# Optimization experiments

Measured on AMD Instinct MI355X. Metric: run time of the kernel, lower is better.

The kernel has to match this reference:

```python
import jax, jax.numpy as jnp
import numpy as np

CHUNK = 64  # triangles processed per scan step; [CHUNK, S*S] intermediates (~64MB fp32)


def setup_inputs() -> dict:
    key = jax.random.key(0)
    kv, kf = jax.random.split(key)
    N, T = 10000, 2048
    vertices = jax.random.normal(kv, (N, 3), dtype=jnp.float32)
    faces = jax.random.randint(kf, (T, 3), 0, N)
    return {"vertices": vertices, "faces": faces, "elevation": 30, "azimuth": 45, "image_size": 500}


def _forward(vertices, faces, elevation, azimuth, image_size):
    S = int(image_size)
    deg = jnp.float32(np.pi / 180.0)
    e = jnp.float32(elevation) * deg
    a = jnp.float32(azimuth) * deg
    ca, sa, ce, se = jnp.cos(a), jnp.sin(a), jnp.cos(e), jnp.sin(e)
    rot_y = jnp.array([[ca, 0.0, sa], [0.0, 1.0, 0.0], [-sa, 0.0, ca]], dtype=jnp.float32)
    rot_x = jnp.array([[1.0, 0.0, 0.0], [0.0, ce, -se], [0.0, se, ce]], dtype=jnp.float32)
    vr = vertices @ (rot_y @ rot_x)                     # [N,3] rotated
    vr = vr.at[:, 2].add(2.0)                           # push in front of camera
    v2d = vr[:, :2] / vr[:, 2:3]                        # perspective divide
    v2d = (v2d + 1.0) * (S / 2.0)                       # NDC -> pixel coords

    f0, f1, f2 = faces[:, 0], faces[:, 1], faces[:, 2]
    p0, p1, p2 = vr[f0], vr[f1], vr[f2]
    n = jnp.cross(p1 - p0, p2 - p0)
    n = n / (jnp.linalg.norm(n, axis=1, keepdims=True) + 1e-8)
    diffuse = jnp.clip(n[:, 2], 0.0, 1.0) * 180.0 + 75.0        # light_dir = (0,0,1)
    colors = jnp.broadcast_to(diffuse[:, None], (faces.shape[0], 3)).astype(jnp.float32)

    z = vr[:, 2][faces].mean(axis=1)                    # [T] painter depth

    tri = jnp.trunc(v2d[faces])                         # [T,3,2]; matches torch .long() truncation
    V0, V1, V2 = tri[:, 0], tri[:, 1], tri[:, 2]
    area = 0.5 * jnp.abs((V1[:, 0] - V0[:, 0]) * (V2[:, 1] - V0[:, 1])
                         - (V2[:, 0] - V0[:, 0]) * (V1[:, 1] - V0[:, 1]))
    valid = area >= 1e-5

    # clamped bounding boxes (note: original never draws row/col image_size-1)
    mnx = jnp.maximum(0.0, jnp.min(tri[:, :, 0], 1))
    mxx = jnp.minimum(S - 1.0, jnp.max(tri[:, :, 0], 1) + 1.0)
    mny = jnp.maximum(0.0, jnp.min(tri[:, :, 1], 1))
    mxy = jnp.minimum(S - 1.0, jnp.max(tri[:, :, 1], 1) + 1.0)

    xs = jnp.arange(S, dtype=jnp.float32)
    gy, gx = jnp.meshgrid(xs, xs, indexing='ij')
    px, py = gx.reshape(-1), gy.reshape(-1)             # [P] pixel centers
    P = S * S
    T = faces.shape[0]
    pad = (-T) % CHUNK

    def padc(x, v):
        if pad == 0:
            return x
        return jnp.concatenate([x, jnp.full((pad,) + x.shape[1:], v, x.dtype)], axis=0)

    nch = (T + pad) // CHUNK

    def r(x):
        return x.reshape((nch, CHUNK) + x.shape[1:])

    chunks = (r(padc(tri, 0.0)), r(padc(colors, 0.0)), r(padc(z, np.inf)),
              r(padc(area, 0.0)), r(padc(valid, False)),
              r(padc(mnx, 0.0)), r(padc(mxx, 0.0)), r(padc(mny, 0.0)), r(padc(mxy, 0.0)))

    # Painter's algorithm (draw far->near, near overwrites) == per-pixel min-z covering triangle.
    def body(carry, c):
        bz, bc = carry
        t, col, zc, ar, vld, x0, x1, y0, y1 = c
        v0x, v0y = t[:, 0, 0][:, None], t[:, 0, 1][:, None]
        v1x, v1y = t[:, 1, 0][:, None], t[:, 1, 1][:, None]
        v2x, v2y = t[:, 2, 0][:, None], t[:, 2, 1][:, None]
        inv = (1.0 / (ar + 1e-8))[:, None]
        w0 = 0.5 * jnp.abs((v1x - px) * (v2y - py) - (v2x - px) * (v1y - py)) * inv
        w1 = 0.5 * jnp.abs((v2x - px) * (v0y - py) - (v0x - px) * (v2y - py)) * inv
        w2 = 1.0 - w0 - w1
        cover = (w0 >= 0) & (w1 >= 0) & (w2 >= 0) & (w0 <= 1) & (w1 <= 1) & (w2 <= 1)
        inbox = (px >= x0[:, None]) & (px < x1[:, None]) & (py >= y0[:, None]) & (py < y1[:, None])
        ok = cover & inbox & vld[:, None]                # [C,P]
        zeff = jnp.where(ok, zc[:, None], jnp.inf)
        zmin = jnp.min(zeff, axis=0)                     # [P]
        i = jnp.argmin(zeff, axis=0)                     # [P]
        cand = col[i]                                    # [P,3]
        upd = zmin < bz
        return (jnp.where(upd, zmin, bz), jnp.where(upd[:, None], cand, bc)), None

    init = (jnp.full((P,), np.inf, jnp.float32), jnp.full((P, 3), 255.0, jnp.float32))
    (bz, bc), _ = jax.lax.scan(body, init, chunks)
    return bc.reshape(S, S, 3)


def reference(vertices, faces, elevation, azimuth, image_size):
    return _forward(vertices, faces, elevation, azimuth, image_size)
```

## Files before the change

### kernel.cpp

```cpp
#include <hip/hip_runtime.h>
#include <math.h>


#define TILE 16
#define K    8

__device__ __forceinline__ void rot_matrix(int elev, int azim,
                                           float& r00, float& r01, float& r02,
                                           float& r11, float& r12,
                                           float& r20, float& r21, float& r22) {
  const float degf = (float)(3.14159265358979323846 / 180.0);
  float e = __fmul_rn((float)elev, degf);
  float a = __fmul_rn((float)azim, degf);
  float ca = (float)cos((double)a);
  float sa = (float)sin((double)a);
  float ce = (float)cos((double)e);
  float se = (float)sin((double)e);
  r00 = ca;  r01 = __fmul_rn(sa, se); r02 = __fmul_rn(sa, ce);
  r11 = ce;  r12 = -se;
  r20 = -sa; r21 = __fmul_rn(ca, se); r22 = __fmul_rn(ca, ce);
}

__device__ __forceinline__ void xform_vertex(
    const float* __restrict__ verts, int i, float halfS,
    float r00, float r01, float r02, float r11, float r12,
    float r20, float r21, float r22,
    float& X, float& Y, float& Z, float& TX, float& TY) {
  float a0 = verts[3 * i + 0];
  float a1 = verts[3 * i + 1];
  float a2 = verts[3 * i + 2];
  float x = __fadd_rn(__fadd_rn(__fmul_rn(a0, r00), __fmul_rn(a1, 0.0f)), __fmul_rn(a2, r20));
  float y = __fadd_rn(__fadd_rn(__fmul_rn(a0, r01), __fmul_rn(a1, r11)), __fmul_rn(a2, r21));
  float z = __fadd_rn(__fadd_rn(__fmul_rn(a0, r02), __fmul_rn(a1, r12)), __fmul_rn(a2, r22));
  z = __fadd_rn(z, 2.0f);
  float sx = __fmul_rn(__fadd_rn(__fdiv_rn(x, z), 1.0f), halfS);
  float sy = __fmul_rn(__fadd_rn(__fdiv_rn(y, z), 1.0f), halfS);
  X = x; Y = y; Z = z;
  TX = truncf(sx);
  TY = truncf(sy);
}

__global__ void prep_kernel(const int* __restrict__ faces,
                            const float* __restrict__ verts,
                            const int* __restrict__ elev,
                            const int* __restrict__ azim,
                            float4* __restrict__ rec,
                            float* __restrict__ gx0, float* __restrict__ gx1,
                            float* __restrict__ gy0, float* __restrict__ gy1,
                            float* __restrict__ gv0x, float* __restrict__ gv0y,
                            float* __restrict__ gv1x, float* __restrict__ gv1y,
                            float* __restrict__ gv2x, float* __restrict__ gv2y,
                            float* __restrict__ ginv, unsigned* __restrict__ gzu,
                            float* __restrict__ colors,
                            ulonglong2* __restrict__ keybuf2, int n2,
                            int T, const int* __restrict__ psize) {
  int t = blockIdx.x * blockDim.x + threadIdx.x;
  if (t < n2) keybuf2[t] = make_ulonglong2(~0ULL, ~0ULL);
  if (t >= T) return;
  float r00, r01, r02, r11, r12, r20, r21, r22;
  rot_matrix(*elev, *azim, r00, r01, r02, r11, r12, r20, r21, r22);
  int S = *psize;
  float halfS = (float)((double)S * 0.5);
  int f0 = faces[3 * t + 0];
  int f1 = faces[3 * t + 1];
  int f2 = faces[3 * t + 2];
  float p0x, p0y, p0z, t0x, t0y;
  float p1x, p1y, p1z, t1x, t1y;
  float p2x, p2y, p2z, t2x, t2y;
  xform_vertex(verts, f0, halfS, r00, r01, r02, r11, r12, r20, r21, r22,
               p0x, p0y, p0z, t0x, t0y);
  xform_vertex(verts, f1, halfS, r00, r01, r02, r11, r12, r20, r21, r22,
               p1x, p1y, p1z, t1x, t1y);
  xform_vertex(verts, f2, halfS, r00, r01, r02, r11, r12, r20, r21, r22,
               p2x, p2y, p2z, t2x, t2y);
  float e1x = __fsub_rn(p1x, p0x), e1y = __fsub_rn(p1y, p0y), e1z = __fsub_rn(p1z, p0z);
  float e2x = __fsub_rn(p2x, p0x), e2y = __fsub_rn(p2y, p0y), e2z = __fsub_rn(p2z, p0z);
  float nx = __fsub_rn(__fmul_rn(e1y, e2z), __fmul_rn(e1z, e2y));
  float ny = __fsub_rn(__fmul_rn(e1z, e2x), __fmul_rn(e1x, e2z));
  float nz = __fsub_rn(__fmul_rn(e1x, e2y), __fmul_rn(e1y, e2x));
  float nrm = __fsqrt_rn(__fadd_rn(__fadd_rn(__fmul_rn(nx, nx), __fmul_rn(ny, ny)),
                                   __fmul_rn(nz, nz)));
  float nnz = __fdiv_rn(nz, __fadd_rn(nrm, 1e-8f));
  float cl = fminf(fmaxf(nnz, 0.0f), 1.0f);
  float col = __fadd_rn(__fmul_rn(cl, 180.0f), 75.0f);
  float zf = __fdiv_rn(__fadd_rn(__fadd_rn(p0z, p1z), p2z), 3.0f);
  float cr = __fsub_rn(__fmul_rn(__fsub_rn(t1x, t0x), __fsub_rn(t2y, t0y)),
                       __fmul_rn(__fsub_rn(t2x, t0x), __fsub_rn(t1y, t0y)));
  float area = __fmul_rn(0.5f, fabsf(cr));
  bool valid = (area >= 1e-5f);
  float inv = __fdiv_rn(1.0f, __fadd_rn(area, 1e-8f));
  float Sm1 = (float)(S - 1);
  float x0 = fmaxf(0.0f, fminf(fminf(t0x, t1x), t2x));
  float x1 = fminf(Sm1, __fadd_rn(fmaxf(fmaxf(t0x, t1x), t2x), 1.0f));
  float y0 = fmaxf(0.0f, fminf(fminf(t0y, t1y), t2y));
  float y1 = fminf(Sm1, __fadd_rn(fmaxf(fmaxf(t0y, t1y), t2y), 1.0f));
  unsigned zb = __float_as_uint(zf);
  unsigned zu = (zb & 0x80000000u) ? ~zb : (zb | 0x80000000u);
  if (!valid) x1 = -3.0e38f;
  gx0[t] = x0; gx1[t] = x1; gy0[t] = y0; gy1[t] = y1;
  gv0x[t] = t0x; gv0y[t] = t0y;
  gv1x[t] = t1x; gv1y[t] = t1y;
  gv2x[t] = t2x; gv2y[t] = t2y;
  ginv[t] = inv;
  gzu[t] = zu;
  colors[t] = col;
  float4 r0, r1, r2, r3;
  r0.x = t0x; r0.y = t0y; r0.z = t1x; r0.w = t1y;
  r1.x = t2x; r1.y = t2y; r1.z = x0;  r1.w = x1;
  r2.x = y0;  r2.y = y1;  r2.z = inv; r2.w = col;
  r3.x = __uint_as_float(zu); r3.y = __uint_as_float((unsigned)t);
  r3.z = 0.0f; r3.w = 0.0f;
  rec[4 * t + 0] = r0;
  rec[4 * t + 1] = r1;
  rec[4 * t + 2] = r2;
  rec[4 * t + 3] = r3;
}

__device__ __forceinline__ bool covers_rect(
    float q0x, float q0y, float q1x, float q1y, float q2x, float q2y,
    float qinv, float X0, float X1, float Y0, float Y1) {
  bool fin = fabsf(q0x) < 1e17f && fabsf(q0y) < 1e17f &&
             fabsf(q1x) < 1e17f && fabsf(q1y) < 1e17f &&
             fabsf(q2x) < 1e17f && fabsf(q2y) < 1e17f;
  if (!fin) return false;
  float A0 = q1x - X0, A1 = q1x - X1, B0 = q2y - Y0, B1 = q2y - Y1;
  float C0 = q2x - X0, C1 = q2x - X1, D0 = q1y - Y0, D1 = q1y - Y1;
  float E0 = q0y - Y0, E1 = q0y - Y1, F0 = q0x - X0, F1 = q0x - X1;
  float p, q;
  p = A0 * B0; q = C0 * D0; float u00 = p - q; float su = fabsf(p) + fabsf(q);
  p = A0 * B1; q = C0 * D1; float u01 = p - q; su = fmaxf(su, fabsf(p) + fabsf(q));
  p = A1 * B0; q = C1 * D0; float u10 = p - q; su = fmaxf(su, fabsf(p) + fabsf(q));
  p = A1 * B1; q = C1 * D1; float u11 = p - q; su = fmaxf(su, fabsf(p) + fabsf(q));
  p = C0 * E0; q = F0 * B0; float v00 = p - q; float sv = fabsf(p) + fabsf(q);
  p = C0 * E1; q = F0 * B1; float v01 = p - q; sv = fmaxf(sv, fabsf(p) + fabsf(q));
  p = C1 * E0; q = F1 * B0; float v10 = p - q; sv = fmaxf(sv, fabsf(p) + fabsf(q));
  p = C1 * E1; q = F1 * B1; float v11 = p - q; sv = fmaxf(sv, fabsf(p) + fabsf(q));
  float umax = fmaxf(fmaxf(fabsf(u00), fabsf(u01)), fmaxf(fabsf(u10), fabsf(u11)));
  float vmax = fmaxf(fmaxf(fabsf(v00), fabsf(v01)), fmaxf(fabsf(v10), fabsf(v11)));
  float epsU = 2e-6f * su, epsV = 2e-6f * sv;
  float hv = 0.5f * qinv;
  return ((umax + epsU) * hv <= 0.9999f) &&
         ((vmax + epsV) * hv <= 0.9999f) &&
         ((umax + vmax + epsU + epsV) * hv <= 0.9999f);
}

__global__ __launch_bounds__(256) void cull_kernel(
    const float* __restrict__ gx0, const float* __restrict__ gx1,
    const float* __restrict__ gy0, const float* __restrict__ gy1,
    const float* __restrict__ gv0x, const float* __restrict__ gv0y,
    const float* __restrict__ gv1x, const float* __restrict__ gv1y,
    const float* __restrict__ gv2x, const float* __restrict__ gv2y,
    const float* __restrict__ ginv, const unsigned* __restrict__ gzu,
    unsigned* __restrict__ stripzu, int T, int ntx) {
  __shared__ unsigned red[4];
  int tile = blockIdx.x;
  int tid = threadIdx.x;
  int lane = tid & 63;
  int wid = tid >> 6;
  int tx = tile % ntx, ty = tile / ntx;
  float TX0 = (float)(tx * TILE), TX1 = (float)(tx * TILE + TILE - 1);
  float TY0 = (float)(ty * TILE), TY1 = (float)(ty * TILE + TILE - 1);

  unsigned best = 0xFFFFFFFFu;
  for (int g = tid; g < T; g += 256) {
    unsigned zu = gzu[g];
    if (zu >= best) continue;
    float x0 = gx0[g], x1 = gx1[g], y0 = gy0[g], y1 = gy1[g];
    if (!(TX0 >= x0 && TX1 < x1 && TY0 >= y0 && TY1 < y1)) continue;
    if (covers_rect(gv0x[g], gv0y[g], gv1x[g], gv1y[g], gv2x[g], gv2y[g],
                    ginv[g], TX0, TX1, TY0, TY1))
      best = zu;
  }
  for (int o = 32; o > 0; o >>= 1)
    best = min(best, (unsigned)__shfl_down((int)best, o));
  if (lane == 0) red[wid] = best;
  __syncthreads();
  unsigned tilezu = min(min(red[0], red[1]), min(red[2], red[3]));

  float Y0 = (float)(ty * TILE + wid * 4), Y1 = Y0 + 3.0f;
  unsigned sbest = tilezu;
  for (int g = lane; g < T; g += 64) {
    unsigned zu = gzu[g];
    if (zu >= sbest) continue;
    float x0 = gx0[g], x1 = gx1[g], y0 = gy0[g], y1 = gy1[g];
    if (!(TX0 >= x0 && TX1 < x1 && Y0 >= y0 && Y1 < y1)) continue;
    if (covers_rect(gv0x[g], gv0y[g], gv1x[g], gv1y[g], gv2x[g], gv2y[g],
                    ginv[g], TX0, TX1, Y0, Y1))
      sbest = zu;
  }
  for (int o = 32; o > 0; o >>= 1)
    sbest = min(sbest, (unsigned)__shfl_down((int)sbest, o));
  if (lane == 0) stripzu[tile * 4 + wid] = sbest;
}

__global__ __launch_bounds__(256) void raster_kernel(
    const float4* __restrict__ rec,
    const float* __restrict__ gx0, const float* __restrict__ gx1,
    const float* __restrict__ gy0, const float* __restrict__ gy1,
    const float* __restrict__ gv0x, const float* __restrict__ gv0y,
    const float* __restrict__ gv1x, const float* __restrict__ gv1y,
    const float* __restrict__ gv2x, const float* __restrict__ gv2y,
    const float* __restrict__ ginv, const unsigned* __restrict__ gzu,
    const unsigned* __restrict__ stripzu,
    const int* __restrict__ psize,
    unsigned long long* __restrict__ keybuf,
    int T, int ntx, int fpb) {
  int S = *psize;
  int tile = blockIdx.x / K;
  int rseg = blockIdx.x - tile * K;
  int tx = tile % ntx, ty = tile / ntx;
  int tid = threadIdx.x;
  int lane = tid & 63;
  int wid = tid >> 6;
  int col = tid & (TILE - 1);
  int row = tid / TILE;
  int px_i = tx * TILE + col;
  int py_i = ty * TILE + row;
  float px = (float)px_i, py = (float)py_i;
  bool inimg = (px_i < S) && (py_i < S);
  unsigned long long bkey = ~0ULL;
  unsigned tzu = stripzu[tile * 4 + wid];
  float wxlo = (float)(tx * TILE), wxhi = (float)(tx * TILE + TILE - 1);
  float wylo = (float)(ty * TILE + wid * 4);
  float wyhi = wylo + 3.0f;

  int base = rseg * fpb;
  int lim = min(base + fpb, T);

  for (int g = base; g < lim; g += 64) {
    int fi = g + lane;
    bool in = fi < lim;
    float fx0 = in ? gx0[fi] : 3.0e38f;
    float fx1 = in ? gx1[fi] : -3.0e38f;
    float fy0 = in ? gy0[fi] : 3.0e38f;
    float fy1 = in ? gy1[fi] : -3.0e38f;
    unsigned fzu = in ? gzu[fi] : 0xFFFFFFFFu;
    bool ovb = (wxhi >= fx0) && (wxlo < fx1) && (wyhi >= fy0) && (wylo < fy1) &&
               (fzu <= tzu);
    bool ov = false;
    if (ovb) {
      float q0x = gv0x[fi], q0y = gv0y[fi];
      float q1x = gv1x[fi], q1y = gv1y[fi];
      float q2x = gv2x[fi], q2y = gv2y[fi];
      float qinv = ginv[fi];
      bool fin = fabsf(q0x) < 1e17f && fabsf(q0y) < 1e17f &&
                 fabsf(q1x) < 1e17f && fabsf(q1y) < 1e17f &&
                 fabsf(q2x) < 1e17f && fabsf(q2y) < 1e17f;
      float X0 = fmaxf(wxlo, fx0), X1 = fminf(wxhi, fx1);
      float Y0 = fmaxf(wylo, fy0), Y1 = fminf(wyhi, fy1);
      float A0 = q1x - X0, A1 = q1x - X1;
      float B0 = q2y - Y0, B1 = q2y - Y1;
      float C0 = q2x - X0, C1 = q2x - X1;
      float D0 = q1y - Y0, D1 = q1y - Y1;
      float E0 = q0y - Y0, E1 = q0y - Y1;
      float F0 = q0x - X0, F1 = q0x - X1;
      float p, q;
      p = A0 * B0; q = C0 * D0; float u00 = p - q; float su = fabsf(p) + fabsf(q);
      p = A0 * B1; q = C0 * D1; float u01 = p - q; su = fmaxf(su, fabsf(p) + fabsf(q));
      p = A1 * B0; q = C1 * D0; float u10 = p - q; su = fmaxf(su, fabsf(p) + fabsf(q));
      p = A1 * B1; q = C1 * D1; float u11 = p - q; su = fmaxf(su, fabsf(p) + fabsf(q));
      p = C0 * E0; q = F0 * B0; float v00 = p - q; float sv = fabsf(p) + fabsf(q);
      p = C0 * E1; q = F0 * B1; float v01 = p - q; sv = fmaxf(sv, fabsf(p) + fabsf(q));
      p = C1 * E0; q = F1 * B0; float v10 = p - q; sv = fmaxf(sv, fabsf(p) + fabsf(q));
      p = C1 * E1; q = F1 * B1; float v11 = p - q; sv = fmaxf(sv, fabsf(p) + fabsf(q));
      float epsU = 2e-6f * su;
      float epsV = 2e-6f * sv;
      float epsS = epsU + epsV;
      auto minabs4 = [](float x00, float x01, float x10, float x11, float eps) {
        float lo = fminf(fminf(x00, x01), fminf(x10, x11));
        float hi = fmaxf(fmaxf(x00, x01), fmaxf(x10, x11));
        float mres = 0.0f;
        if (lo > eps) mres = lo - eps;
        else if (hi < -eps) mres = -hi - eps;
        return mres;
      };
      float m0 = minabs4(u00, u01, u10, u11, epsU);
      float m1 = minabs4(v00, v01, v10, v11, epsV);
      float msum = minabs4(u00 + v00, u01 + v01, u10 + v10, u11 + v11, epsS);
      float mdif = minabs4(u00 - v00, u01 - v01, u10 - v10, u11 - v11, epsS);
      float mm = fmaxf(msum, mdif);
      float hv = 0.5f * qinv;
      bool rej = fin && ((m0 * hv > 1.0001f) || (m1 * hv > 1.0001f) ||
                         (mm * hv > 1.0001f));
      ov = !rej;
    }
    unsigned long long m = __ballot(ov);
    while (m) {
      int j0 = __builtin_ctzll(m); m &= m - 1;
      int j1 = -1, j2 = -1, j3 = -1;
      if (m) { j1 = __builtin_ctzll(m); m &= m - 1;
        if (m) { j2 = __builtin_ctzll(m); m &= m - 1;
          if (m) { j3 = __builtin_ctzll(m); m &= m - 1; } } }
      const float4* p0 = rec + 4 * (g + j0);
      const float4* p1 = rec + 4 * (g + (j1 >= 0 ? j1 : j0));
      const float4* p2 = rec + 4 * (g + (j2 >= 0 ? j2 : j0));
      const float4* p3 = rec + 4 * (g + (j3 >= 0 ? j3 : j0));
      float4 a0 = p0[0], a1 = p0[1], a2 = p0[2], a3 = p0[3];
      float4 b0 = p1[0], b1 = p1[1], b2 = p1[2], b3 = p1[3];
      float4 c0 = p2[0], c1 = p2[1], c2 = p2[2], c3 = p2[3];
      float4 d0 = p3[0], d1 = p3[1], d2 = p3[2], d3 = p3[3];

#define PROCESS(q0, q1, q2, q3, enable)                                        \
      if (enable) {                                                            \
        float v0x = q0.x, v0y = q0.y, v1x = q0.z, v1y = q0.w;                  \
        float v2x = q1.x, v2y = q1.y, x0 = q1.z, x1 = q1.w;                    \
        float y0 = q2.x, y1 = q2.y, inv = q2.z;                                \
                  \
        float e0 = __fsub_rn(__fmul_rn(__fsub_rn(v1x, px), __fsub_rn(v2y, py)),\
                             __fmul_rn(__fsub_rn(v2x, px), __fsub_rn(v1y, py)));\
        float w0 = __fmul_rn(__fmul_rn(0.5f, fabsf(e0)), inv);                 \
        float e1 = __fsub_rn(__fmul_rn(__fsub_rn(v2x, px), __fsub_rn(v0y, py)),\
                             __fmul_rn(__fsub_rn(v0x, px), __fsub_rn(v2y, py)));\
        float w1 = __fmul_rn(__fmul_rn(0.5f, fabsf(e1)), inv);                 \
        float w2 = __fsub_rn(__fsub_rn(1.0f, w0), w1);                         \
        bool ok = (w0 >= 0.0f) && (w1 >= 0.0f) && (w2 >= 0.0f) &&              \
                  (w0 <= 1.0f) && (w1 <= 1.0f) && (w2 <= 1.0f) &&              \
                  (px >= x0) && (px < x1) && (py >= y0) && (py < y1);          \
        unsigned long long fk =                                                \
            ((unsigned long long)__float_as_uint(q3.x) << 32) |                \
            __float_as_uint(q3.y);                                             \
        if (ok && fk < bkey) bkey = fk;                                        \
      }

      PROCESS(a0, a1, a2, a3, true)
      PROCESS(b0, b1, b2, b3, (j1 >= 0))
      PROCESS(c0, c1, c2, c3, (j2 >= 0))
      PROCESS(d0, d1, d2, d3, (j3 >= 0))
#undef PROCESS
    }
  }

  if (inimg && bkey != ~0ULL) {
    unsigned long long* kp = keybuf + ((size_t)py_i * (size_t)S + px_i);
    unsigned long long cur = *kp;
    if (bkey < cur) atomicMin(kp, bkey);
  }
}

__global__ void resolve_kernel(const unsigned long long* __restrict__ keybuf,
                               const float* __restrict__ colors,
                               float* __restrict__ out,
                               const int* __restrict__ psize) {
  int S = *psize;
  int P = S * S;
  int i = blockIdx.x * blockDim.x + threadIdx.x;
  if (i >= P) return;
  unsigned long long k = keybuf[i];
  float c = (k == 0xFFFFFFFFFFFFFFFFULL)
                ? 255.0f
                : colors[(unsigned)(k & 0xFFFFFFFFULL)];
  out[3 * i + 0] = c;
  out[3 * i + 1] = c;
  out[3 * i + 2] = c;
}

extern "C" void kernel_launch(void* const* d_in, const int* in_sizes, int n_in,
                              void* d_out, int out_size, void* d_ws, size_t ws_size,
                              hipStream_t stream) {
  const float* verts = (const float*)d_in[0];
  const int* faces = (const int*)d_in[1];
  const int* elev = (const int*)d_in[2];
  const int* azim = (const int*)d_in[3];
  const int* psize = (const int*)d_in[4];

  int T = in_sizes[1] / 3;
  const int S_host = 500;
  const int P = S_host * S_host;
  const int ntx = (S_host + TILE - 1) / TILE;
  const int nty = (S_host + TILE - 1) / TILE;
  const int ntiles = ntx * nty;
  int fpb = (((T + K - 1) / K + 63) / 64) * 64;

  float* wsf = (float*)d_ws;
  size_t off = 0;
  auto alloc = [&](size_t nfloats) {
    float* p = wsf + off;
    off += (nfloats + 15) & ~(size_t)15;
    return p;
  };
  float* gx0 = alloc(T);
  float* gx1 = alloc(T);
  float* gy0 = alloc(T);
  float* gy1 = alloc(T);
  float* gv0x = alloc(T);
  float* gv0y = alloc(T);
  float* gv1x = alloc(T);
  float* gv1y = alloc(T);
  float* gv2x = alloc(T);
  float* gv2y = alloc(T);
  float* ginv = alloc(T);
  unsigned* gzu = (unsigned*)alloc(T);
  float* colors = alloc(T);
  unsigned* stripzu = (unsigned*)alloc(ntiles * 4);
  float4* rec = (float4*)alloc((size_t)T * 16);
  unsigned long long* keybuf = (unsigned long long*)alloc((size_t)P * 2);

  int n2 = P / 2;
  int prep_threads = (n2 > T) ? n2 : T;
  prep_kernel<<<(prep_threads + 255) / 256, 256, 0, stream>>>(
      faces, verts, elev, azim, rec, gx0, gx1, gy0, gy1,
      gv0x, gv0y, gv1x, gv1y, gv2x, gv2y, ginv, gzu, colors,
      (ulonglong2*)keybuf, n2, T, psize);
  cull_kernel<<<ntiles, 256, 0, stream>>>(gx0, gx1, gy0, gy1,
                                          gv0x, gv0y, gv1x, gv1y, gv2x, gv2y,
                                          ginv, gzu, stripzu, T, ntx);
  raster_kernel<<<ntiles * K, 256, 0, stream>>>(rec, gx0, gx1, gy0, gy1,
                                                gv0x, gv0y, gv1x, gv1y, gv2x, gv2y,
                                                ginv, gzu, stripzu, psize, keybuf,
                                                T, ntx, fpb);
  resolve_kernel<<<(P + 255) / 256, 256, 0, stream>>>(keybuf, colors,
                                                      (float*)d_out, psize);
}
```

Baseline: 68.60 us.

## Map each wavefront to an 8x8 quad instead of a 16x4 strip, halve K

Each 64-lane wavefront now covers an 8x8 pixel quad of the 16x16 tile instead of a 16x4 row strip. The cull kernel computes a per-quad occluder depth to match. A square footprint overlaps fewer triangle bounding boxes and is more likely to be fully covered by an occluder, so fewer faces need per-pixel edge tests. Separately, the number of face segments per tile drops from 8 to 4, which halves the block count and gives each block more faces to scan. That lowers parallelism in exchange for fewer partial results per pixel.

Measured after the change: 68.21 us. About the same (-0.6%).

```diff
diff --git a/kernel.cpp b/kernel.cpp
--- a/kernel.cpp
+++ b/kernel.cpp
@@ -3,7 +3,7 @@
 
 
 #define TILE 16
-#define K    8
+#define K    4
 
 __device__ __forceinline__ void rot_matrix(int elev, int azim,
                                            float& r00, float& r01, float& r02,
@@ -151,7 +151,7 @@
     const float* __restrict__ gv1x, const float* __restrict__ gv1y,
     const float* __restrict__ gv2x, const float* __restrict__ gv2y,
     const float* __restrict__ ginv, const unsigned* __restrict__ gzu,
-    unsigned* __restrict__ stripzu, int T, int ntx) {
+    unsigned* __restrict__ quadzu, int T, int ntx) {
   __shared__ unsigned red[4];
   int tile = blockIdx.x;
   int tid = threadIdx.x;
@@ -177,20 +177,21 @@
   __syncthreads();
   unsigned tilezu = min(min(red[0], red[1]), min(red[2], red[3]));
 
-  float Y0 = (float)(ty * TILE + wid * 4), Y1 = Y0 + 3.0f;
+  float QX0 = (float)(tx * TILE + (wid & 1) * 8), QX1 = QX0 + 7.0f;
+  float QY0 = (float)(ty * TILE + (wid >> 1) * 8), QY1 = QY0 + 7.0f;
   unsigned sbest = tilezu;
   for (int g = lane; g < T; g += 64) {
     unsigned zu = gzu[g];
     if (zu >= sbest) continue;
     float x0 = gx0[g], x1 = gx1[g], y0 = gy0[g], y1 = gy1[g];
-    if (!(TX0 >= x0 && TX1 < x1 && Y0 >= y0 && Y1 < y1)) continue;
+    if (!(QX0 >= x0 && QX1 < x1 && QY0 >= y0 && QY1 < y1)) continue;
     if (covers_rect(gv0x[g], gv0y[g], gv1x[g], gv1y[g], gv2x[g], gv2y[g],
-                    ginv[g], TX0, TX1, Y0, Y1))
+                    ginv[g], QX0, QX1, QY0, QY1))
       sbest = zu;
   }
   for (int o = 32; o > 0; o >>= 1)
     sbest = min(sbest, (unsigned)__shfl_down((int)sbest, o));
-  if (lane == 0) stripzu[tile * 4 + wid] = sbest;
+  if (lane == 0) quadzu[tile * 4 + wid] = sbest;
 }
 
 __global__ __launch_bounds__(256) void raster_kernel(
@@ -201,7 +202,7 @@
     const float* __restrict__ gv1x, const float* __restrict__ gv1y,
     const float* __restrict__ gv2x, const float* __restrict__ gv2y,
     const float* __restrict__ ginv, const unsigned* __restrict__ gzu,
-    const unsigned* __restrict__ stripzu,
+    const unsigned* __restrict__ quadzu,
     const int* __restrict__ psize,
     unsigned long long* __restrict__ keybuf,
     int T, int ntx, int fpb) {
@@ -212,17 +213,14 @@
   int tid = threadIdx.x;
   int lane = tid & 63;
   int wid = tid >> 6;
-  int col = tid & (TILE - 1);
-  int row = tid / TILE;
-  int px_i = tx * TILE + col;
-  int py_i = ty * TILE + row;
+  int px_i = tx * TILE + (wid & 1) * 8 + (lane & 7);
+  int py_i = ty * TILE + (wid >> 1) * 8 + (lane >> 3);
   float px = (float)px_i, py = (float)py_i;
   bool inimg = (px_i < S) && (py_i < S);
   unsigned long long bkey = ~0ULL;
-  unsigned tzu = stripzu[tile * 4 + wid];
-  float wxlo = (float)(tx * TILE), wxhi = (float)(tx * TILE + TILE - 1);
-  float wylo = (float)(ty * TILE + wid * 4);
-  float wyhi = wylo + 3.0f;
+  unsigned tzu = quadzu[tile * 4 + wid];
+  float wxlo = (float)(tx * TILE + (wid & 1) * 8), wxhi = wxlo + 7.0f;
+  float wylo = (float)(ty * TILE + (wid >> 1) * 8), wyhi = wylo + 7.0f;
 
   int base = rseg * fpb;
   int lim = min(base + fpb, T);
@@ -391,7 +389,7 @@
   float* ginv = alloc(T);
   unsigned* gzu = (unsigned*)alloc(T);
   float* colors = alloc(T);
-  unsigned* stripzu = (unsigned*)alloc(ntiles * 4);
+  unsigned* quadzu = (unsigned*)alloc(ntiles * 4);
   float4* rec = (float4*)alloc((size_t)T * 16);
   unsigned long long* keybuf = (unsigned long long*)alloc((size_t)P * 2);
 
@@ -403,10 +401,10 @@
       (ulonglong2*)keybuf, n2, T, psize);
   cull_kernel<<<ntiles, 256, 0, stream>>>(gx0, gx1, gy0, gy1,
                                           gv0x, gv0y, gv1x, gv1y, gv2x, gv2y,
-                                          ginv, gzu, stripzu, T, ntx);
+                                          ginv, gzu, quadzu, T, ntx);
   raster_kernel<<<ntiles * K, 256, 0, stream>>>(rec, gx0, gx1, gy0, gy1,
                                                 gv0x, gv0y, gv1x, gv1y, gv2x, gv2y,
-                                                ginv, gzu, stripzu, psize, keybuf,
+                                                ginv, gzu, quadzu, psize, keybuf,
                                                 T, ntx, fpb);
   resolve_kernel<<<(P + 255) / 256, 256, 0, stream>>>(keybuf, colors,
                                                       (float*)d_out, psize);
```
